# Performance work log

Hardware: AMD Instinct MI355X
Metric: run time of the kernel (lower is better)

## Reference

```python
import jax, jax.numpy as jnp
import numpy as np

B, DIM, T = 8, 512, 4096
INTER = 1536
K = 7
DIL = 1
EPS = 1e-6
LS_INIT = 1e-6


def _ste(x, q):
    # straight-through estimator: forward uses q, gradient flows through x
    return x + jax.lax.stop_gradient(q - x)


def _weight_quant(w):
    # BitNet b1.58 ternary weight quant with per-tensor scale = mean(|w|)
    s = jnp.clip(jnp.mean(jnp.abs(w)), 1e-5, None)
    q = jnp.clip(jnp.round(w / s), -1.0, 1.0) * s
    return _ste(w, q)


def _act_quant(x, axis):
    # per-token int8 absmax quant along `axis`
    s = 127.0 / jnp.clip(jnp.max(jnp.abs(x), axis=axis, keepdims=True), 1e-5, None)
    q = jnp.clip(jnp.round(x * s), -128.0, 127.0) / s
    return _ste(x, q)


def setup_inputs() -> dict:
    key = jax.random.key(0)
    ks = jax.random.split(key, 5)
    return {
        "x": jax.random.normal(ks[0], (B, DIM, T), dtype=jnp.float32),
        "dw_w": jax.random.normal(ks[1], (DIM, 1, K), dtype=jnp.float32) * 0.1,
        "dw_b": jnp.zeros((DIM,), jnp.float32),
        "ln_g": jnp.ones((DIM,), jnp.float32),
        "ln_b": jnp.zeros((DIM,), jnp.float32),
        "w1": jax.random.normal(ks[2], (INTER, DIM), dtype=jnp.float32) * (1.0 / np.sqrt(DIM)),
        "b1": jnp.zeros((INTER,), jnp.float32),
        "w2": jax.random.normal(ks[3], (DIM, INTER), dtype=jnp.float32) * (1.0 / np.sqrt(INTER)),
        "b2": jnp.zeros((DIM,), jnp.float32),
        "gamma": LS_INIT * jnp.ones((DIM,), jnp.float32),
    }


def reference(x, dw_w, dw_b, ln_g, ln_b, w1, b1, w2, b2, gamma):
    residual = x  # [B, DIM, T]
    pad = (K + (DIL - 1) * (K - 1)) // 2
    # quantized depthwise conv1d
    xq = _act_quant(x, axis=1)
    wq = _weight_quant(dw_w)  # [DIM, 1, K]
    y = jax.lax.conv_general_dilated(
        xq, wq, window_strides=(1,), padding=[(pad, pad)],
        rhs_dilation=(DIL,), dimension_numbers=("NCH", "OIH", "NCH"),
        feature_group_count=DIM,
    ) + dw_b[None, :, None]
    y = y.transpose(0, 2, 1)  # [B, T, DIM]
    # LayerNorm over channels
    mu = jnp.mean(y, axis=-1, keepdims=True)
    var = jnp.var(y, axis=-1, keepdims=True)
    y = (y - mu) * jax.lax.rsqrt(var + EPS) * ln_g + ln_b
    # BitLinear 1 -> GELU -> BitLinear 2
    h = jnp.einsum("btc,fc->btf", _act_quant(y, -1), _weight_quant(w1)) + b1
    h = jax.nn.gelu(h, approximate=False)
    o = jnp.einsum("btf,cf->btc", _act_quant(h, -1), _weight_quant(w2)) + b2
    o = gamma * o
    return residual + o.transpose(0, 2, 1)  # [B, DIM, T]
```

## Files before the change

kernel.cpp:

```cpp
#include <hip/hip_runtime.h>
#include <hip/hip_bf16.h>

#define BATCH 8
#define DIM   512
#define TLEN  4096
#define INTER 1536
#define NTOK  (BATCH*TLEN)

#define QH 15.875f
#define DH (1.0f/15.875f)

typedef __attribute__((ext_vector_type(4))) float f32x4;
typedef __attribute__((ext_vector_type(8))) short s16x8;
typedef __attribute__((ext_vector_type(4))) int   i32x4;
typedef signed char i8;

__device__ __forceinline__ float bf2f(short s) {
  unsigned u = ((unsigned)(unsigned short)s) << 16;
  return __uint_as_float(u);
}
__device__ __forceinline__ short f2bf(float f) {
  union { __hip_bfloat16 h; unsigned short u; } cv;
  cv.h = __float2bfloat16(f);
  return (short)cv.u;
}
__device__ __forceinline__ void async16(void* lds, const void* g) {
  __builtin_amdgcn_global_load_lds((const __attribute__((address_space(1))) void*)g,
                                   (__attribute__((address_space(3))) void*)lds, 16, 0, 0);
}
__device__ __forceinline__ float gelu_sig(float h) {
  float e = __builtin_amdgcn_exp2f(-2.4554669f * h);
  return h * __builtin_amdgcn_rcpf(1.f + e);
}

#define VMW(N) asm volatile("s_waitcnt vmcnt(" #N ")" ::: "memory")
#define LKW0() asm volatile("s_waitcnt lgkmcnt(0)" ::: "memory")

__global__ __launch_bounds__(256)
void reduce_abs3_k(const float* __restrict__ w1, const float* __restrict__ w2,
                   const float* __restrict__ dww, float* __restrict__ ws) {
  const int b = blockIdx.x, tid = threadIdx.x;
  const float* w; int n, nb, lb; float* part;
  if (b < 128)      { w = w1;  n = INTER * DIM; nb = 128; lb = b;       part = ws + 16; }
  else if (b < 256) { w = w2;  n = INTER * DIM; nb = 128; lb = b - 128; part = ws + 144; }
  else              { w = dww; n = DIM * 7;     nb = 8;   lb = b - 256; part = ws + 272; }
  float s = 0.f;
  for (int i = lb * 256 + tid; i < n; i += nb * 256) s += fabsf(w[i]);
  #pragma unroll
  for (int off = 32; off; off >>= 1) s += __shfl_xor(s, off);
  __shared__ float ls[4];
  if ((tid & 63) == 0) ls[tid >> 6] = s;
  __syncthreads();
  if (tid == 0) part[lb] = ls[0] + ls[1] + ls[2] + ls[3];
}

__global__ void finalize_scales_k(float* __restrict__ ws) {
  const int tid = threadIdx.x;
  const int seg = tid >> 6, lane = tid & 63;
  float s;
  if (seg == 0)      s = ws[16 + lane] + ws[16 + 64 + lane];
  else if (seg == 1) s = ws[144 + lane] + ws[144 + 64 + lane];
  else               s = (lane < 8) ? ws[272 + lane] : 0.f;
  #pragma unroll
  for (int off = 32; off; off >>= 1) s += __shfl_xor(s, off);
  if (lane == 0) {
    if (seg == 0)      ws[0] = fmaxf(s / 786432.f, 1e-5f);
    else if (seg == 1) ws[1] = fmaxf(s / 786432.f, 1e-5f);
    else               ws[2] = fmaxf(s / 3584.f, 1e-5f);
  }
}

__global__ __launch_bounds__(256)
void quant_w8_both_k(const float* __restrict__ w1, const float* __restrict__ w2,
                     const float* __restrict__ sc,
                     i8* __restrict__ w1q, i8* __restrict__ w2q) {
  const int bid = blockIdx.x;
  if (bid < 3072) {
    int i = bid * 256 + threadIdx.x;
    w1q[i] = (i8)(int)fminf(fmaxf(rintf(w1[i] / sc[0]), -1.f), 1.f);
  } else {
    int i = (bid - 3072) * 256 + threadIdx.x;
    w2q[i] = (i8)(int)fminf(fmaxf(rintf(w2[i] / sc[1]), -1.f), 1.f);
  }
}

__global__ __launch_bounds__(256)
void amax_k(const float* __restrict__ x, float* __restrict__ amax) {
  const int tid = threadIdx.x;
  const int b = blockIdx.y;
  const int t0 = blockIdx.x * 128;
  const int tg = tid & 31, grp = tid >> 5;
  const float* xb = x + ((size_t)b * DIM + grp * 64) * TLEN + t0 + tg * 4;
  f32x4 m = {0.f, 0.f, 0.f, 0.f};
  for (int c = 0; c < 64; ++c) {
    f32x4 v = *(const f32x4*)(xb + (size_t)c * TLEN);
    #pragma unroll
    for (int e = 0; e < 4; ++e) m[e] = fmaxf(m[e], fabsf(v[e]));
  }
  __shared__ f32x4 pm[8][32];
  pm[grp][tg] = m;
  __syncthreads();
  if (tid < 32) {
    f32x4 r = pm[0][tid];
    #pragma unroll
    for (int g = 1; g < 8; ++g)
      #pragma unroll
      for (int e = 0; e < 4; ++e) r[e] = fmaxf(r[e], pm[g][tid][e]);
    *(f32x4*)&amax[(size_t)b * TLEN + t0 + tid * 4] = r;
  }
}

__global__ __launch_bounds__(256)
void conv_ln_quant_k(const float* __restrict__ x, const float* __restrict__ dww,
                     const float* __restrict__ dwb, const float* __restrict__ lng,
                     const float* __restrict__ lnb, const float* __restrict__ amax,
                     const float* __restrict__ scales, i8* __restrict__ yq,
                     float* __restrict__ siy) {
  __shared__ i8   xq[512 * 52];
  __shared__ short ly[32 * 512];
  __shared__ float sx[40], sxi[40];
  const int tid = threadIdx.x;
  const int b = blockIdx.y;
  const int t0 = blockIdx.x * 32;

  if (tid < 40) {
    int tg = t0 - 4 + tid;
    float a = (tg >= 0 && tg < TLEN) ? amax[(size_t)b * TLEN + tg] : 1.f;
    float m = fmaxf(a, 1e-5f);
    sx[tid] = 127.f / m;
    sxi[tid] = m * (1.f / 127.f);
  }
  __syncthreads();

  const bool interior = (t0 >= 4) && (t0 + 36 <= TLEN);
  #pragma unroll 2
  for (int p = 0; p < 20; ++p) {
    const int g = p * 256 + tid;
    const int c = g / 10;
    const int ch = g - c * 10;
    const float* xr = x + ((size_t)b * DIM + c) * TLEN + (t0 - 4) + ch * 4;
    f32x4 L;
    if (interior) {
      L = *(const f32x4*)xr;
    } else {
      #pragma unroll
      for (int e = 0; e < 4; ++e) {
        int tg = t0 - 4 + ch * 4 + e;
        L[e] = (tg >= 0 && tg < TLEN) ? xr[e] : 0.f;
      }
    }
    const f32x4 S = *(const f32x4*)&sx[ch * 4];
    unsigned pk = 0;
    #pragma unroll
    for (int e = 0; e < 4; ++e) {
      int q = (int)rintf(__builtin_amdgcn_fmed3f(L[e] * S[e], -128.f, 127.f));
      pk |= ((unsigned)(q & 255)) << (8 * e);
    }
    *(unsigned*)(xq + c * 52 + ch * 4) = pk;
  }
  __syncthreads();

  {
    const float sdw = scales[2];
    const float rs = 1.f / sdw;
    const int c0 = tid * 2;
    float w0[7], w1v[7];
    #pragma unroll
    for (int k = 0; k < 7; ++k) {
      w0[k]  = fminf(fmaxf(rintf(dww[c0 * 7 + k] * rs), -1.f), 1.f) * sdw;
      w1v[k] = fminf(fmaxf(rintf(dww[c0 * 7 + 7 + k] * rs), -1.f), 1.f) * sdw;
    }
    const float bias0 = dwb[c0], bias1 = dwb[c0 + 1];
    const i8* xr0 = xq + c0 * 52;
    const i8* xr1 = xr0 + 52;

    #define UNPK(src, u, Q) do {                                            \
      const unsigned v_ = *(const unsigned*)((src) + 4 * (u));              \
      const f32x4 SX_ = *(const f32x4*)&sxi[4 * (u)];                       \
      _Pragma("unroll")                                                     \
      for (int e_ = 0; e_ < 4; ++e_)                                        \
        Q[e_] = (float)((int)(v_ << (24 - 8 * e_)) >> 24) * SX_[e_];        \
    } while (0)

    f32x4 A0, A1, A2, B0, B1, B2;
    UNPK(xr0, 0, A0); UNPK(xr0, 1, A1);
    UNPK(xr1, 0, B0); UNPK(xr1, 1, B1);
    #pragma unroll 1
    for (int u = 0; u < 8; ++u) {
      UNPK(xr0, u + 2, A2);
      UNPK(xr1, u + 2, B2);
      #pragma unroll
      for (int s = 0; s < 4; ++s) {
        float a0 = bias0, a1 = bias1;
        #pragma unroll
        for (int k = 0; k < 7; ++k) {
          const int i = s + 1 + k;
          const float qa = (i < 4) ? A0[i & 3] : (i < 8) ? A1[i & 3] : A2[i & 3];
          const float qb = (i < 4) ? B0[i & 3] : (i < 8) ? B1[i & 3] : B2[i & 3];
          a0 += w0[k] * qa;
          a1 += w1v[k] * qb;
        }
        const int t = 4 * u + s;
        unsigned pk = (unsigned)(unsigned short)f2bf(a0) |
                      ((unsigned)(unsigned short)f2bf(a1) << 16);
        *(unsigned*)((char*)ly + t * 1024 + tid * 4) = pk;
      }
      A0 = A1; A1 = A2; B0 = B1; B1 = B2;
    }
    #undef UNPK
  }
  __syncthreads();

  const int lane = tid & 63, w = tid >> 6;
  float gg[8], bb[8];
  #pragma unroll
  for (int j = 0; j < 8; ++j) { gg[j] = lng[lane * 8 + j]; bb[j] = lnb[lane * 8 + j]; }
  #pragma unroll 1
  for (int i = 0; i < 8; ++i) {
    const int t = w * 8 + i;
    s16x8 v = *(const s16x8*)((char*)ly + t * 1024 + lane * 16);
    float f[8];
    float s = 0.f, sq = 0.f;
    #pragma unroll
    for (int j = 0; j < 8; ++j) { f[j] = bf2f(v[j]); s += f[j]; sq += f[j] * f[j]; }
    #pragma unroll
    for (int off = 32; off; off >>= 1) { s += __shfl_xor(s, off); sq += __shfl_xor(sq, off); }
    const float mu = s * (1.f / 512.f);
    const float var = sq * (1.f / 512.f) - mu * mu;
    const float rstd = rsqrtf(var + 1e-6f);
    float amx = 0.f;
    #pragma unroll
    for (int j = 0; j < 8; ++j) {
      f[j] = (f[j] - mu) * rstd * gg[j] + bb[j];
      amx = fmaxf(amx, fabsf(f[j]));
    }
    #pragma unroll
    for (int off = 32; off; off >>= 1) amx = fmaxf(amx, __shfl_xor(amx, off));
    const float m = fmaxf(amx, 1e-5f);
    const float ss = 127.f / m;
    const int tok = b * TLEN + t0 + t;
    if (lane == 0) siy[tok] = m * (1.f / 127.f);
    unsigned lo = 0, hi = 0;
    #pragma unroll
    for (int j = 0; j < 4; ++j) {
      int q = (int)fminf(fmaxf(rintf(f[j] * ss), -128.f), 127.f);
      lo |= ((unsigned)(q & 255)) << (8 * j);
    }
    #pragma unroll
    for (int j = 4; j < 8; ++j) {
      int q = (int)fminf(fmaxf(rintf(f[j] * ss), -128.f), 127.f);
      hi |= ((unsigned)(q & 255)) << (8 * (j - 4));
    }
    uint2 pk; pk.x = lo; pk.y = hi;
    const int tl = t & 7;
    const int ch = (lane >> 1) ^ tl;
    *(uint2*)(yq + (size_t)tok * DIM + ch * 16 + (lane & 1) * 8) = pk;
  }
}

__global__ __launch_bounds__(512, 2)
void fused_ffn_k(const i8* __restrict__ yq, const i8* __restrict__ w1q,
                 const i8* __restrict__ w2q, const float* __restrict__ b1,
                 const float* __restrict__ b2, const float* __restrict__ gamma,
                 const float* __restrict__ siy, const float* __restrict__ scales,
                 const float* __restrict__ x, float* __restrict__ out) {
  __shared__ i8 smem[163840];
  i8* const yql = smem;
  i8* const hql = smem + 65536;
  const int tid = threadIdx.x;
  const int t0 = blockIdx.x * 64;
  const int lane = tid & 63, w = tid >> 6;
  const int lc = lane & 15, lg = lane >> 4;
  const int srow = lane >> 2, schk = lane & 3;
  i8* const myst = smem + 32768 + w * 4096;

  #pragma unroll
  for (int l = 0; l < 4; ++l)
    async16(yql + l * 8192 + tid * 16, yq + (size_t)t0 * DIM + l * 8192 + tid * 16);

  #define STAGE1(s) do {                                                      \
    const int ftp_ = (s) >> 3, kt_ = (s) & 7;                                 \
    _Pragma("unroll")                                                         \
    for (int q_ = 0; q_ < 4; ++q_) {                                          \
      const int rr_ = q_ * 16 + srow;                                         \
      const int sc_ = schk ^ ((rr_ >> 1) & 3);                                \
      async16(myst + q_ * 1024 + lane * 16,                                   \
              w1q + (size_t)(ftp_ * 512 + w * 64 + rr_) * DIM + kt_ * 64 + sc_ * 16); \
    }                                                                         \
  } while (0)

  STAGE1(0);
  asm volatile("" ::: "memory");
  VMW(4);
  __builtin_amdgcn_s_barrier();

  const float sw1 = scales[0];
  float sy[4];
  #pragma unroll
  for (int j = 0; j < 4; ++j) sy[j] = siy[t0 + j * 16 + lc] * sw1;

  i32x4 acc[4][4] = {};
  #pragma unroll 1
  for (int ftp = 0; ftp < 3; ++ftp) {
    #pragma unroll 1
    for (int kt = 0; kt < 8; ++kt) {
      const int s = ftp * 8 + kt;
      VMW(0);
      i32x4 af[4], bf[4];
      #pragma unroll
      for (int i_ = 0; i_ < 4; ++i_) {
        const int ar = i_ * 16 + lc;
        af[i_] = *(const i32x4*)(myst + ar * 64 + ((lg ^ ((ar >> 1) & 3)) << 4));
      }
      #pragma unroll
      for (int j_ = 0; j_ < 4; ++j_) {
        const int tok = j_ * 16 + lc;
        bf[j_] = *(const i32x4*)(yql + tok * 512 + (((kt * 4 + lg) ^ (tok & 7)) << 4));
      }
      LKW0();
      __builtin_amdgcn_sched_barrier(0);
      if (s < 23) STAGE1(s + 1);
      __builtin_amdgcn_s_setprio(1);
      #pragma unroll
      for (int i_ = 0; i_ < 4; ++i_)
        #pragma unroll
        for (int j_ = 0; j_ < 4; ++j_)
          acc[i_][j_] = __builtin_amdgcn_mfma_i32_16x16x64_i8(af[i_], bf[j_],
                                                              acc[i_][j_], 0, 0, 0);
      __builtin_amdgcn_s_setprio(0);
    }
    #pragma unroll
    for (int i_ = 0; i_ < 4; ++i_) {
      const int f0_ = ftp * 512 + w * 64 + i_ * 16 + lg * 4;
      const int cb_ = ftp * 32 + w * 4 + i_;
      float b1v_[4];
      #pragma unroll
      for (int r_ = 0; r_ < 4; ++r_) b1v_[r_] = b1[f0_ + r_];
      #pragma unroll
      for (int j_ = 0; j_ < 4; ++j_) {
        const int tok_ = j_ * 16 + lc;
        unsigned pk_ = 0;
        #pragma unroll
        for (int r_ = 0; r_ < 4; ++r_) {
          float hv_ = fmaf((float)acc[i_][j_][r_], sy[j_], b1v_[r_]);
          float gv_ = gelu_sig(hv_);
          int q_ = (int)rintf(__builtin_amdgcn_fmed3f(gv_ * QH, -128.f, 127.f));
          pk_ |= ((unsigned)(q_ & 255)) << (8 * r_);
          acc[i_][j_][r_] = 0;
        }
        *(unsigned*)(hql + tok_ * 1536 + (((cb_ ^ (tok_ & 7)) << 4) + lg * 4)) = pk_;
      }
    }
  }
  #undef STAGE1
  __syncthreads();

  #define STAGE2(s) do {                                                      \
    _Pragma("unroll")                                                         \
    for (int q_ = 0; q_ < 4; ++q_) {                                          \
      const int rr_ = q_ * 16 + srow;                                         \
      const int sc_ = schk ^ ((rr_ >> 1) & 3);                                \
      async16(myst + q_ * 1024 + lane * 16,                                   \
              w2q + (size_t)(w * 64 + rr_) * INTER + (s) * 64 + sc_ * 16);    \
    }                                                                         \
  } while (0)

  STAGE2(0);
  i32x4 a3[4][4] = {};
  #pragma unroll 1
  for (int s = 0; s < 24; ++s) {
    VMW(0);
    i32x4 af[4], bf[4];
    #pragma unroll
    for (int i_ = 0; i_ < 4; ++i_) {
      const int ar = i_ * 16 + lc;
      af[i_] = *(const i32x4*)(myst + ar * 64 + ((lg ^ ((ar >> 1) & 3)) << 4));
    }
    #pragma unroll
    for (int j_ = 0; j_ < 4; ++j_) {
      const int tok = j_ * 16 + lc;
      bf[j_] = *(const i32x4*)(hql + tok * 1536 + (((s * 4 + lg) ^ (tok & 7)) << 4));
    }
    LKW0();
    __builtin_amdgcn_sched_barrier(0);
    if (s < 23) STAGE2(s + 1);
    __builtin_amdgcn_s_setprio(1);
    #pragma unroll
    for (int i_ = 0; i_ < 4; ++i_)
      #pragma unroll
      for (int j_ = 0; j_ < 4; ++j_)
        a3[i_][j_] = __builtin_amdgcn_mfma_i32_16x16x64_i8(af[i_], bf[j_],
                                                           a3[i_][j_], 0, 0, 0);
    __builtin_amdgcn_s_setprio(0);
  }
  #undef STAGE2

  const float dq = scales[1] * DH;
  #pragma unroll
  for (int i = 0; i < 4; ++i) {
    const int c0 = w * 64 + i * 16 + lg * 4;
    #pragma unroll
    for (int j = 0; j < 4; ++j) {
      const int tok = t0 + j * 16 + lc;
      const int bb = tok >> 12;
      const int tt = tok & 4095;
      #pragma unroll
      for (int r = 0; r < 4; ++r) {
        const int c = c0 + r;
        float o = (float)a3[i][j][r] * dq + b2[c];
        size_t idx = ((size_t)(bb * DIM + c)) * TLEN + tt;
        out[idx] = x[idx] + gamma[c] * o;
      }
    }
  }
}

extern "C" void kernel_launch(void* const* d_in, const int* in_sizes, int n_in,
                              void* d_out, int out_size, void* d_ws, size_t ws_size,
                              hipStream_t stream) {
  const float* x    = (const float*)d_in[0];
  const float* dww  = (const float*)d_in[1];
  const float* dwb  = (const float*)d_in[2];
  const float* lng  = (const float*)d_in[3];
  const float* lnb  = (const float*)d_in[4];
  const float* w1   = (const float*)d_in[5];
  const float* b1   = (const float*)d_in[6];
  const float* w2   = (const float*)d_in[7];
  const float* b2   = (const float*)d_in[8];
  const float* gam  = (const float*)d_in[9];
  float* out = (float*)d_out;

  const size_t NEEDED = 18616320;
  if (ws_size < NEEDED) return;

  char* ws = (char*)d_ws;
  float* scales = (float*)ws;
  float* amax   = (float*)(ws + 4096);
  float* siy    = (float*)(ws + 135168);
  i8* w1q       = (i8*)(ws + 266240);
  i8* w2q       = (i8*)(ws + 1052672);
  i8* yq        = (i8*)(ws + 1839104);

  reduce_abs3_k<<<264, 256, 0, stream>>>(w1, w2, dww, scales);
  finalize_scales_k<<<1, 192, 0, stream>>>(scales);
  quant_w8_both_k<<<6144, 256, 0, stream>>>(w1, w2, scales, w1q, w2q);
  amax_k<<<dim3(TLEN / 128, BATCH), 256, 0, stream>>>(x, amax);
  conv_ln_quant_k<<<dim3(TLEN / 32, BATCH), 256, 0, stream>>>(x, dww, dwb, lng, lnb,
                                                              amax, scales, yq, siy);
  fused_ffn_k<<<NTOK / 64, 512, 0, stream>>>(yq, w1q, w2q, b1, b2, gam, siy,
                                             scales, x, out);
}
```

Baseline: 173.0 us.

## Fuse amax into conv kernel and coalesce FFN epilogue via bf16 residual pass

Removes the separate amax kernel. The conv/LN kernel now stages raw fp32 x in shared memory, computes the per-token absmax itself, and quantizes on the fly, using 512 threads with one channel per thread. The FFN epilogue transposes results through LDS and writes gamma*o as bf16 with coalesced row stores. A new elementwise kernel then adds the residual x. This trades the uncoalesced strided fp32 stores and an extra read of x for an extra bf16 intermediate round trip and one more launch, with a small precision loss in the bf16 rounding of the scaled FFN output.

```diff
diff --git a/kernel.cpp b/kernel.cpp
--- a/kernel.cpp
+++ b/kernel.cpp
@@ -84,58 +84,24 @@
   }
 }
 
-__global__ __launch_bounds__(256)
-void amax_k(const float* __restrict__ x, float* __restrict__ amax) {
-  const int tid = threadIdx.x;
-  const int b = blockIdx.y;
-  const int t0 = blockIdx.x * 128;
-  const int tg = tid & 31, grp = tid >> 5;
-  const float* xb = x + ((size_t)b * DIM + grp * 64) * TLEN + t0 + tg * 4;
-  f32x4 m = {0.f, 0.f, 0.f, 0.f};
-  for (int c = 0; c < 64; ++c) {
-    f32x4 v = *(const f32x4*)(xb + (size_t)c * TLEN);
-    #pragma unroll
-    for (int e = 0; e < 4; ++e) m[e] = fmaxf(m[e], fabsf(v[e]));
-  }
-  __shared__ f32x4 pm[8][32];
-  pm[grp][tg] = m;
-  __syncthreads();
-  if (tid < 32) {
-    f32x4 r = pm[0][tid];
-    #pragma unroll
-    for (int g = 1; g < 8; ++g)
-      #pragma unroll
-      for (int e = 0; e < 4; ++e) r[e] = fmaxf(r[e], pm[g][tid][e]);
-    *(f32x4*)&amax[(size_t)b * TLEN + t0 + tid * 4] = r;
-  }
-}
-
-__global__ __launch_bounds__(256)
+__global__ __launch_bounds__(512)
 void conv_ln_quant_k(const float* __restrict__ x, const float* __restrict__ dww,
                      const float* __restrict__ dwb, const float* __restrict__ lng,
-                     const float* __restrict__ lnb, const float* __restrict__ amax,
+                     const float* __restrict__ lnb,
                      const float* __restrict__ scales, i8* __restrict__ yq,
                      float* __restrict__ siy) {
-  __shared__ i8   xq[512 * 52];
+  __shared__ float ax[512 * 41];
   __shared__ short ly[32 * 512];
   __shared__ float sx[40], sxi[40];
   const int tid = threadIdx.x;
   const int b = blockIdx.y;
   const int t0 = blockIdx.x * 32;
-
-  if (tid < 40) {
-    int tg = t0 - 4 + tid;
-    float a = (tg >= 0 && tg < TLEN) ? amax[(size_t)b * TLEN + tg] : 1.f;
-    float m = fmaxf(a, 1e-5f);
-    sx[tid] = 127.f / m;
-    sxi[tid] = m * (1.f / 127.f);
-  }
-  __syncthreads();
+  const int lane = tid & 63, w = tid >> 6;
 
   const bool interior = (t0 >= 4) && (t0 + 36 <= TLEN);
   #pragma unroll 2
-  for (int p = 0; p < 20; ++p) {
-    const int g = p * 256 + tid;
+  for (int p = 0; p < 10; ++p) {
+    const int g = p * 512 + tid;
     const int c = g / 10;
     const int ch = g - c * 10;
     const float* xr = x + ((size_t)b * DIM + c) * TLEN + (t0 - 4) + ch * 4;
@@ -149,75 +115,78 @@
         L[e] = (tg >= 0 && tg < TLEN) ? xr[e] : 0.f;
       }
     }
-    const f32x4 S = *(const f32x4*)&sx[ch * 4];
-    unsigned pk = 0;
-    #pragma unroll
-    for (int e = 0; e < 4; ++e) {
-      int q = (int)rintf(__builtin_amdgcn_fmed3f(L[e] * S[e], -128.f, 127.f));
-      pk |= ((unsigned)(q & 255)) << (8 * e);
-    }
-    *(unsigned*)(xq + c * 52 + ch * 4) = pk;
+    #pragma unroll
+    for (int e = 0; e < 4; ++e) ax[c * 41 + ch * 4 + e] = L[e];
+  }
+  __syncthreads();
+
+  if (w < 5) {
+    const int j = w * 8 + (lane & 7);
+    const int cg = lane >> 3;
+    float m = 0.f;
+    #pragma unroll 4
+    for (int cc = 0; cc < 64; ++cc)
+      m = fmaxf(m, fabsf(ax[(cg + 8 * cc) * 41 + j]));
+    m = fmaxf(m, __shfl_xor(m, 8));
+    m = fmaxf(m, __shfl_xor(m, 16));
+    m = fmaxf(m, __shfl_xor(m, 32));
+    if (cg == 0) {
+      int tg = t0 - 4 + j;
+      float a = (tg >= 0 && tg < TLEN) ? fmaxf(m, 1e-5f) : 1.f;
+      sx[j] = 127.f / a;
+      sxi[j] = a * (1.f / 127.f);
+    }
   }
   __syncthreads();
 
   {
     const float sdw = scales[2];
     const float rs = 1.f / sdw;
-    const int c0 = tid * 2;
-    float w0[7], w1v[7];
-    #pragma unroll
-    for (int k = 0; k < 7; ++k) {
-      w0[k]  = fminf(fmaxf(rintf(dww[c0 * 7 + k] * rs), -1.f), 1.f) * sdw;
-      w1v[k] = fminf(fmaxf(rintf(dww[c0 * 7 + 7 + k] * rs), -1.f), 1.f) * sdw;
-    }
-    const float bias0 = dwb[c0], bias1 = dwb[c0 + 1];
-    const i8* xr0 = xq + c0 * 52;
-    const i8* xr1 = xr0 + 52;
-
-    #define UNPK(src, u, Q) do {                                            \
-      const unsigned v_ = *(const unsigned*)((src) + 4 * (u));              \
-      const f32x4 SX_ = *(const f32x4*)&sxi[4 * (u)];                       \
+    const int c = tid;
+    float wv[7];
+    #pragma unroll
+    for (int k = 0; k < 7; ++k)
+      wv[k] = fminf(fmaxf(rintf(dww[c * 7 + k] * rs), -1.f), 1.f) * sdw;
+    const float bias = dwb[c];
+    const float* xr = ax + c * 41;
+
+    #define UNPKQ(u, Q) do {                                                \
       _Pragma("unroll")                                                     \
-      for (int e_ = 0; e_ < 4; ++e_)                                        \
-        Q[e_] = (float)((int)(v_ << (24 - 8 * e_)) >> 24) * SX_[e_];        \
+      for (int e_ = 0; e_ < 4; ++e_) {                                      \
+        const int j_ = 4 * (u) + e_;                                        \
+        Q[e_] = fminf(fmaxf(rintf(xr[j_] * sx[j_]), -128.f), 127.f) * sxi[j_]; \
+      }                                                                     \
     } while (0)
 
-    f32x4 A0, A1, A2, B0, B1, B2;
-    UNPK(xr0, 0, A0); UNPK(xr0, 1, A1);
-    UNPK(xr1, 0, B0); UNPK(xr1, 1, B1);
+    f32x4 A0, A1, A2;
+    UNPKQ(0, A0); UNPKQ(1, A1);
     #pragma unroll 1
     for (int u = 0; u < 8; ++u) {
-      UNPK(xr0, u + 2, A2);
-      UNPK(xr1, u + 2, B2);
+      UNPKQ(u + 2, A2);
       #pragma unroll
       for (int s = 0; s < 4; ++s) {
-        float a0 = bias0, a1 = bias1;
+        float a0 = bias;
         #pragma unroll
         for (int k = 0; k < 7; ++k) {
           const int i = s + 1 + k;
           const float qa = (i < 4) ? A0[i & 3] : (i < 8) ? A1[i & 3] : A2[i & 3];
-          const float qb = (i < 4) ? B0[i & 3] : (i < 8) ? B1[i & 3] : B2[i & 3];
-          a0 += w0[k] * qa;
-          a1 += w1v[k] * qb;
+          a0 += wv[k] * qa;
         }
         const int t = 4 * u + s;
-        unsigned pk = (unsigned)(unsigned short)f2bf(a0) |
-                      ((unsigned)(unsigned short)f2bf(a1) << 16);
-        *(unsigned*)((char*)ly + t * 1024 + tid * 4) = pk;
-      }
-      A0 = A1; A1 = A2; B0 = B1; B1 = B2;
-    }
-    #undef UNPK
-  }
-  __syncthreads();
-
-  const int lane = tid & 63, w = tid >> 6;
+        *(short*)((char*)ly + t * 1024 + c * 2) = f2bf(a0);
+      }
+      A0 = A1; A1 = A2;
+    }
+    #undef UNPKQ
+  }
+  __syncthreads();
+
   float gg[8], bb[8];
   #pragma unroll
   for (int j = 0; j < 8; ++j) { gg[j] = lng[lane * 8 + j]; bb[j] = lnb[lane * 8 + j]; }
   #pragma unroll 1
-  for (int i = 0; i < 8; ++i) {
-    const int t = w * 8 + i;
+  for (int i = 0; i < 4; ++i) {
+    const int t = w * 4 + i;
     s16x8 v = *(const s16x8*)((char*)ly + t * 1024 + lane * 16);
     float f[8];
     float s = 0.f, sq = 0.f;
@@ -263,7 +232,7 @@
                  const i8* __restrict__ w2q, const float* __restrict__ b1,
                  const float* __restrict__ b2, const float* __restrict__ gamma,
                  const float* __restrict__ siy, const float* __restrict__ scales,
-                 const float* __restrict__ x, float* __restrict__ out) {
+                 short* __restrict__ o_out) {
   __shared__ i8 smem[163840];
   i8* const yql = smem;
   i8* const hql = smem + 65536;
@@ -395,24 +364,56 @@
   }
   #undef STAGE2
 
+  __syncthreads();
+  short* const tb = (short*)(hql + w * 4608);
   const float dq = scales[1] * DH;
-  #pragma unroll
-  for (int i = 0; i < 4; ++i) {
-    const int c0 = w * 64 + i * 16 + lg * 4;
-    #pragma unroll
-    for (int j = 0; j < 4; ++j) {
-      const int tok = t0 + j * 16 + lc;
-      const int bb = tok >> 12;
-      const int tt = tok & 4095;
-      #pragma unroll
-      for (int r = 0; r < 4; ++r) {
-        const int c = c0 + r;
-        float o = (float)a3[i][j][r] * dq + b2[c];
-        size_t idx = ((size_t)(bb * DIM + c)) * TLEN + tt;
-        out[idx] = x[idx] + gamma[c] * o;
-      }
-    }
-  }
+  const int bb = t0 >> 12;
+  const int tt0 = t0 & 4095;
+  #pragma unroll 1
+  for (int cp = 0; cp < 2; ++cp) {
+    #pragma unroll
+    for (int ii = 0; ii < 2; ++ii) {
+      const int i = cp * 2 + ii;
+      #pragma unroll
+      for (int j = 0; j < 4; ++j) {
+        const int t = j * 16 + lc;
+        #pragma unroll
+        for (int r = 0; r < 4; ++r) {
+          const int cl = ii * 16 + lg * 4 + r;
+          const int c = w * 64 + cp * 32 + cl;
+          float o = (float)a3[i][j][r] * dq + b2[c];
+          tb[cl * 72 + t] = f2bf(gamma[c] * o);
+        }
+      }
+    }
+    LKW0();
+    #pragma unroll
+    for (int pp = 0; pp < 4; ++pp) {
+      const int row = pp * 8 + (lane >> 3);
+      const int tof = (lane & 7) * 8;
+      s16x8 v = *(const s16x8*)(tb + row * 72 + tof);
+      const int c = w * 64 + cp * 32 + row;
+      *(s16x8*)(o_out + ((size_t)(bb * DIM + c)) * TLEN + tt0 + tof) = v;
+    }
+    LKW0();
+  }
+}
+
+__global__ __launch_bounds__(256)
+void residual_k(const float* __restrict__ x, const short* __restrict__ o,
+                float* __restrict__ out) {
+  const size_t i = ((size_t)blockIdx.x * 256 + threadIdx.x) * 8;
+  s16x8 ov = *(const s16x8*)(o + i);
+  f32x4 a = *(const f32x4*)(x + i);
+  f32x4 b = *(const f32x4*)(x + i + 4);
+  f32x4 r0, r1;
+  #pragma unroll
+  for (int e = 0; e < 4; ++e) {
+    r0[e] = a[e] + bf2f(ov[e]);
+    r1[e] = b[e] + bf2f(ov[e + 4]);
+  }
+  *(f32x4*)(out + i) = r0;
+  *(f32x4*)(out + i + 4) = r1;
 }
 
 extern "C" void kernel_launch(void* const* d_in, const int* in_sizes, int n_in,
@@ -430,23 +431,23 @@
   const float* gam  = (const float*)d_in[9];
   float* out = (float*)d_out;
 
-  const size_t NEEDED = 18616320;
+  const size_t NEEDED = 52170752;
   if (ws_size < NEEDED) return;
 
   char* ws = (char*)d_ws;
   float* scales = (float*)ws;
-  float* amax   = (float*)(ws + 4096);
   float* siy    = (float*)(ws + 135168);
   i8* w1q       = (i8*)(ws + 266240);
   i8* w2q       = (i8*)(ws + 1052672);
   i8* yq        = (i8*)(ws + 1839104);
+  short* obuf   = (short*)(ws + 18616320);
 
   reduce_abs3_k<<<264, 256, 0, stream>>>(w1, w2, dww, scales);
   finalize_scales_k<<<1, 192, 0, stream>>>(scales);
   quant_w8_both_k<<<6144, 256, 0, stream>>>(w1, w2, scales, w1q, w2q);
-  amax_k<<<dim3(TLEN / 128, BATCH), 256, 0, stream>>>(x, amax);
-  conv_ln_quant_k<<<dim3(TLEN / 32, BATCH), 256, 0, stream>>>(x, dww, dwb, lng, lnb,
-                                                              amax, scales, yq, siy);
+  conv_ln_quant_k<<<dim3(TLEN / 32, BATCH), 512, 0, stream>>>(x, dww, dwb, lng, lnb,
+                                                              scales, yq, siy);
   fused_ffn_k<<<NTOK / 64, 512, 0, stream>>>(yq, w1q, w2q, b1, b2, gam, siy,
-                                             scales, x, out);
-}
+                                             scales, obuf);
+  residual_k<<<(NTOK * DIM) / (256 * 8), 256, 0, stream>>>(x, obuf, out);
+}
```

After: 217.3 us. 1.26x slower.
